# Kernel tuning notes

Measured on AMD Instinct MI355X. Metric: run time of the kernel, lower is better.

Reference implementation:

```python
import jax, jax.numpy as jnp
import numpy as np

LAYER_SHAPES = [(256, 64, 56, 56), (256, 128, 28, 28), (256, 256, 14, 14), (256, 512, 7, 7)]
NUM_REF = 2000


def _lid_layer(ref, q, k):
    """MLE LID estimate (Ma et al.) per query row.
    ref: [R, C] reference activations; q: [B, C] pooled query activations.
    """
    # Euclidean cdist via the expansion ||q||^2 - 2 q.ref^T + ||ref||^2
    d2 = (jnp.sum(q * q, axis=1, keepdims=True)
          - 2.0 * (q @ ref.T)
          + jnp.sum(ref * ref, axis=1)[None, :])            # [B, R]
    d = jnp.sqrt(jnp.maximum(d2, 0.0))
    # smallest k+1 distances, drop the nearest (mirrors sorted[:,1:k+1])
    neg_topk = jax.lax.top_k(-d, k + 1)[0]                   # descending in -d => ascending d
    dk = -neg_topk[:, 1:k + 1]                               # [B, k], ascending
    # LID = -k / sum_i log(d_i / d_k)
    return -k / jnp.sum(jnp.log(dk / dk[:, -1:]), axis=1)    # [B]


def setup_inputs() -> dict:
    key = jax.random.key(0)
    ks = jax.random.split(key, 12)
    inp = {}
    for i, shp in enumerate(LAYER_SHAPES):
        inp[f"feat{i}"] = jax.random.normal(ks[i], shp, dtype=jnp.float32)
        inp[f"ref{i}"] = jax.random.normal(ks[4 + i], (NUM_REF, shp[1]), dtype=jnp.float32)
    inp["reg_w"] = jax.random.normal(ks[8], (1, 4), dtype=jnp.float32)
    inp["reg_b"] = jax.random.normal(ks[9], (1,), dtype=jnp.float32)
    inp["k"] = 20
    return inp


def reference(feat0, feat1, feat2, feat3, ref0, ref1, ref2, ref3, reg_w, reg_b, k):
    feats = [feat0, feat1, feat2, feat3]
    refs = [ref0, ref1, ref2, ref3]
    lid_scores = []
    for f, r in zip(feats, refs):
        fq = jnp.mean(f.reshape(f.shape[0], f.shape[1], -1), axis=2)  # [B, C]
        lid_scores.append(_lid_layer(r, fq, k))
    lid_feat = jnp.stack(lid_scores, axis=1)                 # [B, num_layers]
    logit = lid_feat @ reg_w.T + reg_b                        # [B, 1]
    return jax.nn.sigmoid(logit)[:, 0]
```

## Files before the change

kernel.cpp:

```cpp
#include <hip/hip_runtime.h>
#include <cmath>

#define WS_FQ_OFF      0u
#define WS_R2_OFF      245760u
#define WS_LID_OFF     253760u
#define WS_G_OFF       262144u
#define G_CHUNK_STRIDE 512000u
#define NREF           2000
#define KC             64

__global__ __launch_bounds__(256) void pool_kernel(const float* __restrict__ feat,
                                                   float* __restrict__ fq,
                                                   int HW, float invHW) {
    int w = threadIdx.x >> 6, lane = threadIdx.x & 63;
    size_t row = (size_t)blockIdx.x * 4 + w;
    const float* p = feat + row * (size_t)HW;
    float s = 0.f;
    if ((HW & 3) == 0) {
        const float4* p4 = (const float4*)p;
        int n4 = HW >> 2;
        for (int i = lane; i < n4; i += 64) {
            float4 v = p4[i];
            s += (v.x + v.y) + (v.z + v.w);
        }
    } else {
        for (int i = lane; i < HW; i += 64) s += p[i];
    }
    #pragma unroll
    for (int off = 32; off; off >>= 1) s += __shfl_down(s, off, 64);
    if (lane == 0) fq[row] = s * invHW;
}

__global__ __launch_bounds__(256) void r2_kernel(const float* __restrict__ ref0,
                                                 const float* __restrict__ ref1,
                                                 const float* __restrict__ ref2,
                                                 const float* __restrict__ ref3,
                                                 float* __restrict__ r2_all) {
    int layer = blockIdx.y;
    int w = threadIdx.x >> 6, lane = threadIdx.x & 63;
    int r = blockIdx.x * 4 + w;
    if (r >= NREF) return;
    const float* rp; int C;
    switch (layer) {
        case 0:  rp = ref0; C = 64;  break;
        case 1:  rp = ref1; C = 128; break;
        case 2:  rp = ref2; C = 256; break;
        default: rp = ref3; C = 512; break;
    }
    const float4* row = (const float4*)(rp + (size_t)r * C);
    int n4 = C >> 2;
    float s = 0.f;
    for (int i = lane; i < n4; i += 64) {
        float4 v = row[i];
        s += v.x*v.x + v.y*v.y + v.z*v.z + v.w*v.w;
    }
    #pragma unroll
    for (int off = 32; off; off >>= 1) s += __shfl_down(s, off, 64);
    if (lane == 0) r2_all[layer * NREF + r] = s;
}

#define BM 64
#define BN 64
#define BK 32
#define LDT 68
__global__ __launch_bounds__(256) void gemm_qr(const float* __restrict__ A,
                                               const float* __restrict__ B,
                                               float* __restrict__ Gp,
                                               int K, int N) {
    __shared__ __align__(16) float As[BK * LDT];
    __shared__ __align__(16) float Bs[BK * LDT];
    int t = threadIdx.x;
    int tq = t & 15, tr = t >> 4;
    int m0 = blockIdx.x * BM;
    int n0 = blockIdx.y * BN;
    int kb = blockIdx.z * KC;
    int row0 = t >> 3;
    int kc4  = t & 7;
    float acc[4][4] = {};

    for (int k0 = kb; k0 < kb + KC; k0 += BK) {
        #pragma unroll
        for (int half = 0; half < 2; ++half) {
            int row = row0 + half * 32;
            float4 av = *(const float4*)(A + (size_t)(m0 + row) * K + k0 + kc4 * 4);
            int brow = n0 + row;
            float4 bv = make_float4(0.f, 0.f, 0.f, 0.f);
            if (brow < N) bv = *(const float4*)(B + (size_t)brow * K + k0 + kc4 * 4);
            As[(kc4*4 + 0) * LDT + row] = av.x;
            As[(kc4*4 + 1) * LDT + row] = av.y;
            As[(kc4*4 + 2) * LDT + row] = av.z;
            As[(kc4*4 + 3) * LDT + row] = av.w;
            Bs[(kc4*4 + 0) * LDT + row] = bv.x;
            Bs[(kc4*4 + 1) * LDT + row] = bv.y;
            Bs[(kc4*4 + 2) * LDT + row] = bv.z;
            Bs[(kc4*4 + 3) * LDT + row] = bv.w;
        }
        __syncthreads();
        #pragma unroll
        for (int kk = 0; kk < BK; ++kk) {
            float4 a = *(const float4*)&As[kk * LDT + tq * 4];
            float4 b = *(const float4*)&Bs[kk * LDT + tr * 4];
            acc[0][0] += a.x*b.x; acc[0][1] += a.x*b.y; acc[0][2] += a.x*b.z; acc[0][3] += a.x*b.w;
            acc[1][0] += a.y*b.x; acc[1][1] += a.y*b.y; acc[1][2] += a.y*b.z; acc[1][3] += a.y*b.w;
            acc[2][0] += a.z*b.x; acc[2][1] += a.z*b.y; acc[2][2] += a.z*b.z; acc[2][3] += a.z*b.w;
            acc[3][0] += a.w*b.x; acc[3][1] += a.w*b.y; acc[3][2] += a.w*b.z; acc[3][3] += a.w*b.w;
        }
        __syncthreads();
    }

    float* Gout = Gp + (size_t)blockIdx.z * G_CHUNK_STRIDE;
    int rbase = n0 + tr * 4;
    if (rbase < N) {
        #pragma unroll
        for (int i = 0; i < 4; ++i) {
            float4 o = make_float4(acc[i][0], acc[i][1], acc[i][2], acc[i][3]);
            *(float4*)(Gout + (size_t)(m0 + tq*4 + i) * N + rbase) = o;
        }
    }
}

__global__ __launch_bounds__(256) void topk_lid_kernel(const float* __restrict__ fq_all,
                                                       const float* __restrict__ G_all,
                                                       const float* __restrict__ r2_all,
                                                       float* __restrict__ lid,
                                                       const int* __restrict__ kptr) {
    __shared__ __align__(16) float d2s[NREF];
    __shared__ unsigned hist[2048];
    __shared__ float redq[4], redm[4], redl[4];
    __shared__ unsigned long long red8[4];
    __shared__ int sh_B, sh_cbelow, sh_cnt;
    __shared__ float sh_dmin;

    const int Cs[4]   = {64, 128, 256, 512};
    const int fqo[4]  = {0, 16384, 49152, 114688};
    const int nchs[4] = {1, 2, 4, 8};
    const int coff[4] = {0, 1, 3, 7};

    int b = blockIdx.x, layer = blockIdx.y;
    int t = threadIdx.x;
    int lane = t & 63, w = t >> 6;
    int k = kptr[0];
    if (k + 1 > NREF) k = NREF - 1;
    unsigned K1 = (unsigned)(k + 1);
    int C = Cs[layer];
    int nch = nchs[layer];
    const float* fq = fq_all + fqo[layer] + (size_t)b * C;
    const float* Gb = G_all + (size_t)coff[layer] * G_CHUNK_STRIDE + (size_t)b * NREF;
    const float* r2 = r2_all + layer * NREF;
    const float INF = __uint_as_float(0x7f800000u);

    for (int i = t; i < 2048; i += 256) hist[i] = 0u;
    if (t == 0) sh_cnt = 0;
    float s = 0.f;
    for (int c = t; c < C; c += 256) { float v = fq[c]; s += v * v; }
    #pragma unroll
    for (int off = 32; off; off >>= 1) s += __shfl_down(s, off, 64);
    if (lane == 0) redq[w] = s;
    __syncthreads();
    float q2 = redq[0] + redq[1] + redq[2] + redq[3];

    float minv = INF;
    for (int i = t; i < NREF / 4; i += 256) {
        float4 g = make_float4(0.f, 0.f, 0.f, 0.f);
        for (int c = 0; c < nch; ++c) {
            float4 v = *(const float4*)(Gb + (size_t)c * G_CHUNK_STRIDE + i * 4);
            g.x += v.x; g.y += v.y; g.z += v.z; g.w += v.w;
        }
        float4 rr = *(const float4*)(r2 + i * 4);
        float d0 = q2 - 2.f * g.x + rr.x; d0 = d0 > 0.f ? d0 : 0.f;
        float d1 = q2 - 2.f * g.y + rr.y; d1 = d1 > 0.f ? d1 : 0.f;
        float d2_ = q2 - 2.f * g.z + rr.z; d2_ = d2_ > 0.f ? d2_ : 0.f;
        float d3 = q2 - 2.f * g.w + rr.w; d3 = d3 > 0.f ? d3 : 0.f;
        *(float4*)(d2s + i * 4) = make_float4(d0, d1, d2_, d3);
        atomicAdd(&hist[__float_as_uint(d0) >> 20], 1u);
        atomicAdd(&hist[__float_as_uint(d1) >> 20], 1u);
        atomicAdd(&hist[__float_as_uint(d2_) >> 20], 1u);
        atomicAdd(&hist[__float_as_uint(d3) >> 20], 1u);
        minv = fminf(minv, fminf(fminf(d0, d1), fminf(d2_, d3)));
    }
    #pragma unroll
    for (int off = 32; off; off >>= 1) minv = fminf(minv, __shfl_down(minv, off, 64));
    if (lane == 0) redm[w] = minv;
    __syncthreads();

    if (t < 64) {
        unsigned p = 0;
        int base = t * 32;
        #pragma unroll 4
        for (int i = 0; i < 32; ++i) p += hist[base + i];
        unsigned cum = p;
        #pragma unroll
        for (int off = 1; off < 64; off <<= 1) {
            unsigned o = __shfl_up(cum, off, 64);
            if (t >= off) cum += o;
        }
        unsigned excl = cum - p;
        if (excl < K1 && K1 <= cum) {
            unsigned run = excl;
            int binB = base;
            for (int i = 0; i < 32; ++i) {
                unsigned c = hist[base + i];
                if (run + c >= K1) { binB = base + i; break; }
                run += c;
            }
            sh_B = binB;
            sh_cbelow = (int)run;
        }
        if (t == 0) sh_dmin = fminf(fminf(redm[0], redm[1]), fminf(redm[2], redm[3]));
    }
    __syncthreads();

    int B = sh_B;
    float* cand = (float*)hist;
    float lsum = 0.f;
    for (int i = t; i < NREF; i += 256) {
        float v = d2s[i];
        int bin = (int)(__float_as_uint(v) >> 20);
        if (bin < B) {
            lsum += logf(v);
        } else if (bin == B) {
            int pos = atomicAdd(&sh_cnt, 1);
            cand[pos] = v;
        }
    }
    #pragma unroll
    for (int off = 32; off; off >>= 1) lsum += __shfl_down(lsum, off, 64);
    if (lane == 0) redl[w] = lsum;
    __syncthreads();

    int cnt = sh_cnt;
    int m = (int)K1 - sh_cbelow;
    if (cnt <= 64) {
        if (t < 64) {
            float mv = (t < cnt) ? cand[t] : INF;
            float csum = 0.f, dk = 0.f;
            for (int it = 0; it < m; ++it) {
                float x = mv;
                #pragma unroll
                for (int off = 32; off; off >>= 1) x = fminf(x, __shfl_xor(x, off, 64));
                csum += logf(x);
                dk = x;
                unsigned long long ball = __ballot(mv == x);
                int src = __ffsll(ball) - 1;
                if (t == src) mv = INF;
            }
            if (t == 0) {
                float lsum_tot = redl[0] + redl[1] + redl[2] + redl[3];
                float denom = 0.5f * (lsum_tot + csum - logf(sh_dmin) - (float)k * logf(dk));
                lid[b * 4 + layer] = -(float)k / denom;
            }
        }
    } else {
        float csum = 0.f, dk = 0.f;
        for (int it = 0; it < m; ++it) {
            unsigned long long best = ~0ull;
            for (int i = t; i < cnt; i += 256) {
                unsigned long long key =
                    ((unsigned long long)__float_as_uint(cand[i]) << 32) | (unsigned)i;
                if (key < best) best = key;
            }
            #pragma unroll
            for (int off = 32; off; off >>= 1) {
                unsigned long long o = __shfl_down(best, off, 64);
                if (o < best) best = o;
            }
            if (lane == 0) red8[w] = best;
            __syncthreads();
            unsigned long long mm = red8[0];
            #pragma unroll
            for (int ww = 1; ww < 4; ++ww) if (red8[ww] < mm) mm = red8[ww];
            float v = __uint_as_float((unsigned)(mm >> 32));
            if (t == 0) {
                csum += logf(v);
                dk = v;
                cand[(int)(mm & 0xffffffffu)] = INF;
            }
            __syncthreads();
        }
        if (t == 0) {
            float lsum_tot = redl[0] + redl[1] + redl[2] + redl[3];
            float denom = 0.5f * (lsum_tot + csum - logf(sh_dmin) - (float)k * logf(dk));
            lid[b * 4 + layer] = -(float)k / denom;
        }
    }
}

__global__ __launch_bounds__(256) void head_kernel(const float* __restrict__ lid,
                                                   const float* __restrict__ w,
                                                   const float* __restrict__ bias,
                                                   float* __restrict__ out) {
    int b = threadIdx.x;
    float acc = bias[0];
    #pragma unroll
    for (int l = 0; l < 4; ++l) acc += lid[b * 4 + l] * w[l];
    out[b] = 1.f / (1.f + expf(-acc));
}

extern "C" void kernel_launch(void* const* d_in, const int* in_sizes, int n_in,
                              void* d_out, int out_size, void* d_ws, size_t ws_size,
                              hipStream_t stream) {
    const float* feat[4] = {(const float*)d_in[0], (const float*)d_in[2],
                            (const float*)d_in[4], (const float*)d_in[6]};
    const float* ref[4]  = {(const float*)d_in[1], (const float*)d_in[3],
                            (const float*)d_in[5], (const float*)d_in[7]};
    const float* reg_w = (const float*)d_in[8];
    const float* reg_b = (const float*)d_in[9];
    const int*   kptr  = (const int*)d_in[10];

    float* ws     = (float*)d_ws;
    float* fq_all = ws + WS_FQ_OFF;
    float* r2_all = ws + WS_R2_OFF;
    float* lid    = ws + WS_LID_OFF;
    float* G_part = ws + WS_G_OFF;

    const int Cs[4]   = {64, 128, 256, 512};
    const int HWs[4]  = {3136, 784, 196, 49};
    const int fqo[4]  = {0, 16384, 49152, 114688};
    const int coff[4] = {0, 1, 3, 7};

    for (int l = 0; l < 4; ++l) {
        int rows = 256 * Cs[l];
        pool_kernel<<<rows / 4, 256, 0, stream>>>(feat[l], fq_all + fqo[l],
                                                  HWs[l], 1.0f / (float)HWs[l]);
    }
    r2_kernel<<<dim3(NREF / 4, 4), 256, 0, stream>>>(ref[0], ref[1], ref[2], ref[3], r2_all);
    for (int l = 0; l < 4; ++l) {
        int chunks = Cs[l] / KC;
        gemm_qr<<<dim3(256 / BM, (NREF + BN - 1) / BN, chunks), 256, 0, stream>>>(
            fq_all + fqo[l], ref[l], G_part + (size_t)coff[l] * G_CHUNK_STRIDE, Cs[l], NREF);
    }
    topk_lid_kernel<<<dim3(256, 4), 256, 0, stream>>>(fq_all, G_part, r2_all, lid, kptr);
    head_kernel<<<1, 256, 0, stream>>>(lid, reg_w, reg_b, (float*)d_out);
}
```

Before: 479.6 us.

## Merge pooling, ref-norm, and per-layer GEMM launches into fewer fused kernels

Combines the four pool launches and the r2 launch into one kernel that dispatches on block index, and replaces four split-K GEMM launches with a single launch that indexes the layer by blockIdx.z and runs the full K loop. The top-k kernel now reads one G value per reference instead of summing K-chunk partials. This cuts launch count and partial-sum traffic, at the cost of less GEMM parallelism for the larger-K layers (fewer blocks doing longer loops), which can leave the GPU underfilled with only 4x32x4 blocks.

```diff
diff --git a/kernel.cpp b/kernel.cpp
--- a/kernel.cpp
+++ b/kernel.cpp
@@ -5,87 +5,110 @@
 #define WS_R2_OFF      245760u
 #define WS_LID_OFF     253760u
 #define WS_G_OFF       262144u
-#define G_CHUNK_STRIDE 512000u
+#define G_LAYER_STRIDE 512000u
 #define NREF           2000
-#define KC             64
-
-__global__ __launch_bounds__(256) void pool_kernel(const float* __restrict__ feat,
-                                                   float* __restrict__ fq,
-                                                   int HW, float invHW) {
+
+#define POOL_BLOCKS 61440
+__global__ __launch_bounds__(256) void pool_r2_kernel(const float* __restrict__ f0,
+                                                      const float* __restrict__ f1,
+                                                      const float* __restrict__ f2,
+                                                      const float* __restrict__ f3,
+                                                      const float* __restrict__ r0,
+                                                      const float* __restrict__ r1,
+                                                      const float* __restrict__ r2p,
+                                                      const float* __restrict__ r3,
+                                                      float* __restrict__ fq_all,
+                                                      float* __restrict__ r2_all) {
+    int blk = blockIdx.x;
     int w = threadIdx.x >> 6, lane = threadIdx.x & 63;
-    size_t row = (size_t)blockIdx.x * 4 + w;
-    const float* p = feat + row * (size_t)HW;
-    float s = 0.f;
-    if ((HW & 3) == 0) {
-        const float4* p4 = (const float4*)p;
-        int n4 = HW >> 2;
+
+    if (blk < POOL_BLOCKS) {
+        const float* feat; int HW; int fqo; int lblk;
+        if (blk < 4096)        { feat = f0; HW = 3136; fqo = 0;      lblk = blk;         }
+        else if (blk < 12288)  { feat = f1; HW = 784;  fqo = 16384;  lblk = blk - 4096;  }
+        else if (blk < 28672)  { feat = f2; HW = 196;  fqo = 49152;  lblk = blk - 12288; }
+        else                   { feat = f3; HW = 49;   fqo = 114688; lblk = blk - 28672; }
+        size_t row = (size_t)lblk * 4 + w;
+        const float* p = feat + row * (size_t)HW;
+        float s = 0.f;
+        if ((HW & 3) == 0) {
+            const float4* p4 = (const float4*)p;
+            int n4 = HW >> 2;
+            for (int i = lane; i < n4; i += 64) {
+                float4 v = p4[i];
+                s += (v.x + v.y) + (v.z + v.w);
+            }
+        } else {
+            for (int i = lane; i < HW; i += 64) s += p[i];
+        }
+        #pragma unroll
+        for (int off = 32; off; off >>= 1) s += __shfl_down(s, off, 64);
+        if (lane == 0) fq_all[fqo + row] = s * (1.0f / (float)HW);
+    } else {
+        int rb = blk - POOL_BLOCKS;
+        int layer = rb / 500;
+        int r = (rb % 500) * 4 + w;
+        if (r >= NREF) return;
+        const float* rp; int C;
+        switch (layer) {
+            case 0:  rp = r0;  C = 64;  break;
+            case 1:  rp = r1;  C = 128; break;
+            case 2:  rp = r2p; C = 256; break;
+            default: rp = r3;  C = 512; break;
+        }
+        const float4* rowp = (const float4*)(rp + (size_t)r * C);
+        int n4 = C >> 2;
+        float s = 0.f;
         for (int i = lane; i < n4; i += 64) {
-            float4 v = p4[i];
-            s += (v.x + v.y) + (v.z + v.w);
-        }
-    } else {
-        for (int i = lane; i < HW; i += 64) s += p[i];
-    }
-    #pragma unroll
-    for (int off = 32; off; off >>= 1) s += __shfl_down(s, off, 64);
-    if (lane == 0) fq[row] = s * invHW;
-}
-
-__global__ __launch_bounds__(256) void r2_kernel(const float* __restrict__ ref0,
-                                                 const float* __restrict__ ref1,
-                                                 const float* __restrict__ ref2,
-                                                 const float* __restrict__ ref3,
-                                                 float* __restrict__ r2_all) {
-    int layer = blockIdx.y;
-    int w = threadIdx.x >> 6, lane = threadIdx.x & 63;
-    int r = blockIdx.x * 4 + w;
-    if (r >= NREF) return;
-    const float* rp; int C;
-    switch (layer) {
-        case 0:  rp = ref0; C = 64;  break;
-        case 1:  rp = ref1; C = 128; break;
-        case 2:  rp = ref2; C = 256; break;
-        default: rp = ref3; C = 512; break;
-    }
-    const float4* row = (const float4*)(rp + (size_t)r * C);
-    int n4 = C >> 2;
-    float s = 0.f;
-    for (int i = lane; i < n4; i += 64) {
-        float4 v = row[i];
-        s += v.x*v.x + v.y*v.y + v.z*v.z + v.w*v.w;
-    }
-    #pragma unroll
-    for (int off = 32; off; off >>= 1) s += __shfl_down(s, off, 64);
-    if (lane == 0) r2_all[layer * NREF + r] = s;
+            float4 v = rowp[i];
+            s += v.x*v.x + v.y*v.y + v.z*v.z + v.w*v.w;
+        }
+        #pragma unroll
+        for (int off = 32; off; off >>= 1) s += __shfl_down(s, off, 64);
+        if (lane == 0) r2_all[layer * NREF + r] = s;
+    }
 }
 
 #define BM 64
 #define BN 64
 #define BK 32
 #define LDT 68
-__global__ __launch_bounds__(256) void gemm_qr(const float* __restrict__ A,
-                                               const float* __restrict__ B,
-                                               float* __restrict__ Gp,
-                                               int K, int N) {
+__global__ __launch_bounds__(256) void gemm_all(const float* __restrict__ fq_all,
+                                                const float* __restrict__ ref0,
+                                                const float* __restrict__ ref1,
+                                                const float* __restrict__ ref2,
+                                                const float* __restrict__ ref3,
+                                                float* __restrict__ G) {
     __shared__ __align__(16) float As[BK * LDT];
     __shared__ __align__(16) float Bs[BK * LDT];
+    int layer = blockIdx.z;
+    const float* B; int K;
+    switch (layer) {
+        case 0:  B = ref0; K = 64;  break;
+        case 1:  B = ref1; K = 128; break;
+        case 2:  B = ref2; K = 256; break;
+        default: B = ref3; K = 512; break;
+    }
+    const int fqo[4] = {0, 16384, 49152, 114688};
+    const float* A = fq_all + fqo[layer];
+    float* Gout = G + (size_t)layer * G_LAYER_STRIDE;
+
     int t = threadIdx.x;
     int tq = t & 15, tr = t >> 4;
     int m0 = blockIdx.x * BM;
     int n0 = blockIdx.y * BN;
-    int kb = blockIdx.z * KC;
     int row0 = t >> 3;
     int kc4  = t & 7;
     float acc[4][4] = {};
 
-    for (int k0 = kb; k0 < kb + KC; k0 += BK) {
+    for (int k0 = 0; k0 < K; k0 += BK) {
         #pragma unroll
         for (int half = 0; half < 2; ++half) {
             int row = row0 + half * 32;
             float4 av = *(const float4*)(A + (size_t)(m0 + row) * K + k0 + kc4 * 4);
             int brow = n0 + row;
             float4 bv = make_float4(0.f, 0.f, 0.f, 0.f);
-            if (brow < N) bv = *(const float4*)(B + (size_t)brow * K + k0 + kc4 * 4);
+            if (brow < NREF) bv = *(const float4*)(B + (size_t)brow * K + k0 + kc4 * 4);
             As[(kc4*4 + 0) * LDT + row] = av.x;
             As[(kc4*4 + 1) * LDT + row] = av.y;
             As[(kc4*4 + 2) * LDT + row] = av.z;
@@ -108,13 +131,12 @@
         __syncthreads();
     }
 
-    float* Gout = Gp + (size_t)blockIdx.z * G_CHUNK_STRIDE;
     int rbase = n0 + tr * 4;
-    if (rbase < N) {
+    if (rbase < NREF) {
         #pragma unroll
         for (int i = 0; i < 4; ++i) {
             float4 o = make_float4(acc[i][0], acc[i][1], acc[i][2], acc[i][3]);
-            *(float4*)(Gout + (size_t)(m0 + tq*4 + i) * N + rbase) = o;
+            *(float4*)(Gout + (size_t)(m0 + tq*4 + i) * NREF + rbase) = o;
         }
     }
 }
@@ -133,8 +155,6 @@
 
     const int Cs[4]   = {64, 128, 256, 512};
     const int fqo[4]  = {0, 16384, 49152, 114688};
-    const int nchs[4] = {1, 2, 4, 8};
-    const int coff[4] = {0, 1, 3, 7};
 
     int b = blockIdx.x, layer = blockIdx.y;
     int t = threadIdx.x;
@@ -143,9 +163,8 @@
     if (k + 1 > NREF) k = NREF - 1;
     unsigned K1 = (unsigned)(k + 1);
     int C = Cs[layer];
-    int nch = nchs[layer];
     const float* fq = fq_all + fqo[layer] + (size_t)b * C;
-    const float* Gb = G_all + (size_t)coff[layer] * G_CHUNK_STRIDE + (size_t)b * NREF;
+    const float* Gb = G_all + (size_t)layer * G_LAYER_STRIDE + (size_t)b * NREF;
     const float* r2 = r2_all + layer * NREF;
     const float INF = __uint_as_float(0x7f800000u);
 
@@ -161,11 +180,7 @@
 
     float minv = INF;
     for (int i = t; i < NREF / 4; i += 256) {
-        float4 g = make_float4(0.f, 0.f, 0.f, 0.f);
-        for (int c = 0; c < nch; ++c) {
-            float4 v = *(const float4*)(Gb + (size_t)c * G_CHUNK_STRIDE + i * 4);
-            g.x += v.x; g.y += v.y; g.z += v.z; g.w += v.w;
-        }
+        float4 g = *(const float4*)(Gb + i * 4);
         float4 rr = *(const float4*)(r2 + i * 4);
         float d0 = q2 - 2.f * g.x + rr.x; d0 = d0 > 0.f ? d0 : 0.f;
         float d1 = q2 - 2.f * g.y + rr.y; d1 = d1 > 0.f ? d1 : 0.f;
@@ -311,24 +326,17 @@
     float* fq_all = ws + WS_FQ_OFF;
     float* r2_all = ws + WS_R2_OFF;
     float* lid    = ws + WS_LID_OFF;
-    float* G_part = ws + WS_G_OFF;
-
-    const int Cs[4]   = {64, 128, 256, 512};
-    const int HWs[4]  = {3136, 784, 196, 49};
-    const int fqo[4]  = {0, 16384, 49152, 114688};
-    const int coff[4] = {0, 1, 3, 7};
-
-    for (int l = 0; l < 4; ++l) {
-        int rows = 256 * Cs[l];
-        pool_kernel<<<rows / 4, 256, 0, stream>>>(feat[l], fq_all + fqo[l],
-                                                  HWs[l], 1.0f / (float)HWs[l]);
-    }
-    r2_kernel<<<dim3(NREF / 4, 4), 256, 0, stream>>>(ref[0], ref[1], ref[2], ref[3], r2_all);
-    for (int l = 0; l < 4; ++l) {
-        int chunks = Cs[l] / KC;
-        gemm_qr<<<dim3(256 / BM, (NREF + BN - 1) / BN, chunks), 256, 0, stream>>>(
-            fq_all + fqo[l], ref[l], G_part + (size_t)coff[l] * G_CHUNK_STRIDE, Cs[l], NREF);
-    }
-    topk_lid_kernel<<<dim3(256, 4), 256, 0, stream>>>(fq_all, G_part, r2_all, lid, kptr);
+    float* G      = ws + WS_G_OFF;
+
+    pool_r2_kernel<<<POOL_BLOCKS + 2000, 256, 0, stream>>>(
+        feat[0], feat[1], feat[2], feat[3],
+        ref[0], ref[1], ref[2], ref[3],
+        fq_all, r2_all);
+
+    gemm_all<<<dim3(256 / BM, (NREF + BN - 1) / BN, 4), 256, 0, stream>>>(
+        fq_all, ref[0], ref[1], ref[2], ref[3], G);
+
+    topk_lid_kernel<<<dim3(256, 4), 256, 0, stream>>>(fq_all, G, r2_all, lid, kptr);
+
     head_kernel<<<1, 256, 0, stream>>>(lid, reg_w, reg_b, (float*)d_out);
 }
```

Result: no change. 472.6 us (-1.5%).
